# Optimization experiments

Hardware: AMD Instinct MI355X
Metric: run time of the kernel (lower is better)

## Reference

```python
import jax, jax.numpy as jnp
import numpy as np

MAX_ANGLES = 6
SCALES = 2
BN_EPS = 1e-5


def _gauss(k):
    # Gaussian filter init used by WaveletTransform1D (kernel_size k, sigma=k/4)
    xs = np.arange(k, dtype=np.float32) - k // 2
    w = np.exp(-xs ** 2 / (2.0 * (k / 4.0) ** 2)).astype(np.float32)
    return jnp.asarray((w / w.sum()).reshape(1, 1, k))


def setup_inputs():
    key = jax.random.key(0)
    ks = jax.random.split(key, 8)
    B, C, H, W = 8, 64, 128, 128
    return {
        "x": jax.random.normal(ks[0], (B, C, H, W), jnp.float32),
        "lin1_w": jax.random.normal(ks[1], (32, C * 16), jnp.float32) * 0.02,
        "lin1_b": jnp.zeros((32,), jnp.float32),
        "lin2_w": jax.random.normal(ks[2], (MAX_ANGLES, 32), jnp.float32) * 0.02,
        "lin2_b": jnp.zeros((MAX_ANGLES,), jnp.float32),
        "wf0": _gauss(3),
        "wf1": _gauss(5),
        "fuse_w": jax.random.normal(ks[3], (C, C * SCALES), jnp.float32) * 0.05,
        "fuse_b": jax.random.normal(ks[4], (C,), jnp.float32) * 0.05,
        "bn_gamma": jnp.ones((C,), jnp.float32),
        "bn_beta": jnp.zeros((C,), jnp.float32),
        "bn_mean": jnp.zeros((C,), jnp.float32),
        "bn_var": jnp.ones((C,), jnp.float32),
    }


def _grid_sample(img, grid):
    # torch F.grid_sample, bilinear, align_corners=True, padding_mode='zeros'
    N, C, H, W = img.shape
    ix = (grid[..., 0] + 1.0) * 0.5 * (W - 1)  # (N,Hg,Wg)
    iy = (grid[..., 1] + 1.0) * 0.5 * (H - 1)
    x0 = jnp.floor(ix)
    y0 = jnp.floor(iy)
    wx = ix - x0
    wy = iy - y0

    def gather(xi, yi):
        valid = (xi >= 0) & (xi <= W - 1) & (yi >= 0) & (yi <= H - 1)
        xc = jnp.clip(xi, 0, W - 1).astype(jnp.int32)
        yc = jnp.clip(yi, 0, H - 1).astype(jnp.int32)
        v = jax.vmap(lambda im, yy, xx: im[:, yy, xx])(img, yc, xc)  # (N,C,Hg,Wg)
        return v * valid[:, None, :, :].astype(img.dtype)

    v00 = gather(x0, y0)
    v01 = gather(x0 + 1, y0)
    v10 = gather(x0, y0 + 1)
    v11 = gather(x0 + 1, y0 + 1)
    return (v00 * ((1 - wx) * (1 - wy))[:, None]
            + v01 * (wx * (1 - wy))[:, None]
            + v10 * ((1 - wx) * wy)[:, None]
            + v11 * (wx * wy)[:, None])


def _interp1d(x, Lout):
    # F.interpolate mode='linear', align_corners=False, over last axis
    Lin = x.shape[-1]
    real = jnp.clip((jnp.arange(Lout, dtype=jnp.float32) + 0.5) * (Lin / Lout) - 0.5, 0.0, Lin - 1.0)
    i0 = jnp.floor(real).astype(jnp.int32)
    i1 = jnp.minimum(i0 + 1, Lin - 1)
    w = real - i0
    return x[..., i0] * (1.0 - w) + x[..., i1] * w


def _interp_last_ac(x, Lout):
    # linear interp over last axis, align_corners=True
    Lin = x.shape[-1]
    if Lin == Lout:
        return x
    pos = jnp.arange(Lout, dtype=jnp.float32) * ((Lin - 1) / (Lout - 1))
    i0 = jnp.floor(pos).astype(jnp.int32)
    i1 = jnp.minimum(i0 + 1, Lin - 1)
    w = pos - i0
    return x[..., i0] * (1.0 - w) + x[..., i1] * w


def _avgpool1(x):
    L = x.shape[-1]
    return x[..., : (L // 2) * 2].reshape(x.shape[:-1] + (L // 2, 2)).mean(-1)


def _conv1(sig, w):
    # sig (N,1,L), w (1,1,k), 'same' padding cross-correlation (matches torch Conv1d)
    k = w.shape[-1]
    return jax.lax.conv_general_dilated(sig, w, (1,), [(k // 2, k // 2)],
                                        dimension_numbers=("NCH", "OIH", "NCH"))


def reference(x, lin1_w, lin1_b, lin2_w, lin2_b, wf0, wf1, fuse_w, fuse_b,
              bn_gamma, bn_beta, bn_mean, bn_var):
    B, C, H, W = x.shape
    K = MAX_ANGLES
    # --- AnglePredictor: adaptive avg pool 4x4 (H,W divisible by 4) + MLP ---
    pooled = x.reshape(B, C, 4, H // 4, 4, W // 4).mean(axis=(3, 5))  # (B,C,4,4)
    feat = pooled.reshape(B, C * 16)
    h = jax.nn.relu(feat @ lin1_w.T + lin1_b)
    off = (h @ lin2_w.T + lin2_b) * 30.0
    base = jnp.linspace(0.0, 180.0, K)
    angles = jnp.sort(jnp.clip(base[None, :] + off, 0.0, 180.0), axis=1)  # (B,K)
    # --- RadonTransform: per-angle rotation grid + grid_sample + sum over W ---
    xs = jnp.linspace(-1.0, 1.0, W)
    ys = jnp.linspace(-1.0, 1.0, H)
    yc, xc = jnp.meshgrid(ys, xs, indexing="ij")
    th = angles * (jnp.pi / 180.0)
    co = jnp.cos(th)[:, :, None, None]
    si = jnp.sin(th)[:, :, None, None]
    gx = xc[None, None] * co + yc[None, None] * si
    gy = -xc[None, None] * si + yc[None, None] * co
    grid = jnp.stack([gx, gy], axis=-1).reshape(B * K, H, W, 2)
    xexp = jnp.broadcast_to(x[:, None], (B, K, C, H, W)).reshape(B * K, C, H, W)
    rotated = _grid_sample(xexp, grid)          # (B*K,C,H,W)
    sig = rotated.sum(axis=3)                   # (B*K,C,H) == sinogram permuted
    # --- WaveletTransform1D (2 scales, L=H=128 > 4) ---
    N = B * K
    c0 = _conv1(sig.reshape(N * C, 1, H), wf0).reshape(N, C, H)
    cur = _avgpool1(sig)                        # (N,C,H//2)
    L2 = H // 2
    f1 = _conv1(cur.reshape(N * C, 1, L2), wf1)
    u1 = _interp1d(_avgpool1(f1), L2).reshape(N, C, L2)
    c1 = _interp1d(u1, H)                       # resized to target length H
    coeffs = jnp.stack([c0, c1], axis=2)        # (N,C,SCALES,H)
    wav = coeffs.reshape(B, K, C, SCALES, H).transpose(0, 2, 4, 3, 1)  # (B,C,H,S,K)
    combined = wav.reshape(B, C * SCALES, H, K)  # matches torch .view on contiguous
    # --- bilinear align_corners=True resize (H,K)->(H,W), separable ---
    combined = _interp_last_ac(combined, W)
    combined = _interp_last_ac(combined.swapaxes(-1, -2), H).swapaxes(-1, -2)
    # --- fusion: 1x1 conv + BatchNorm(eval) + ReLU ---
    out = jnp.einsum("oc,bchw->bohw", fuse_w, combined) + fuse_b[None, :, None, None]
    scale = (bn_gamma / jnp.sqrt(bn_var + BN_EPS))[None, :, None, None]
    out = (out - bn_mean[None, :, None, None]) * scale + bn_beta[None, :, None, None]
    return jax.nn.relu(out)
```

## Files before the change

kernel.cpp:

```cpp
#include <hip/hip_runtime.h>
#include <hip/hip_fp16.h>
#include <math.h>

#define BB 8
#define CC 64
#define HH 128
#define WW 128
#define KK 6

#define FEAT_OFF 0
#define COEF_OFF 8192

#define WSTR 133
#define NROW 132
#define IMGW (NROW * WSTR)
#define IBASE (2 * WSTR + 2)

typedef __fp16   h2  __attribute__((ext_vector_type(2)));
typedef _Float16 hf2 __attribute__((ext_vector_type(2)));

#if __has_builtin(__builtin_amdgcn_fdot2)
#define FDOT2(A, B) __builtin_amdgcn_fdot2(__builtin_bit_cast(hf2, (A)), \
                                           __builtin_bit_cast(hf2, (B)), 0.f, false)
#define FDOT2A(A, B, C) __builtin_amdgcn_fdot2(__builtin_bit_cast(hf2, (A)), \
                                               __builtin_bit_cast(hf2, (B)), (C), false)
#define HAVE_FDOT2 1
#endif

__global__ __launch_bounds__(256) void k_pool(const float* __restrict__ x,
                                              float* __restrict__ ws) {
    int bc = blockIdx.x;
    int b = bc >> 6, c = bc & 63;
    int t = threadIdx.x;
    __shared__ float pool_l[16];
    if (t < 16) pool_l[t] = 0.f;
    __syncthreads();
    const float4* img4 = (const float4*)(x + (size_t)bc * 16384);
    float acc[4] = {0.f, 0.f, 0.f, 0.f};
    int cb = (t & 31) >> 3;
    #pragma unroll
    for (int r = 0; r < 16; ++r) {
        float4 v = img4[r * 256 + t];
        acc[r >> 2] += (v.x + v.y) + (v.z + v.w);
    }
    #pragma unroll
    for (int rb = 0; rb < 4; ++rb)
        atomicAdd(&pool_l[rb * 4 + cb], acc[rb]);
    __syncthreads();
    if (t < 16)
        ws[FEAT_OFF + b * 1024 + c * 16 + t] = pool_l[t] * (1.0f / 1024.0f);
}

#ifdef HAVE_FDOT2
#define SAMPLED(RR, CC, ACC) do {                                  \
    float fr_ = floorf(RR), fc_ = floorf(CC);                      \
    float wr_ = (RR) - fr_, wc_ = (CC) - fc_;                      \
    h2 wv_ = __builtin_amdgcn_cvt_pkrtz(1.0f - wc_, wc_);          \
    int idx_ = IBASE + (int)fmaf(fr_, 133.f, fc_);                 \
    h2 tp_ = imgh[idx_];                                           \
    h2 bt_ = imgh[idx_ + WSTR];                                    \
    float top_ = FDOT2(wv_, tp_);                                  \
    float d_ = FDOT2A(wv_, bt_, -top_);                            \
    ACC = fmaf(wr_, d_, ACC + top_);                               \
} while (0)
#else
#define SAMPLED(RR, CC, ACC) do {                                  \
    float fr_ = floorf(RR), fc_ = floorf(CC);                      \
    float wr_ = (RR) - fr_, wc_ = (CC) - fc_;                      \
    int idx_ = IBASE + (int)fmaf(fr_, 133.f, fc_);                 \
    h2 tp_ = imgh[idx_];                                           \
    h2 bt_ = imgh[idx_ + WSTR];                                    \
    float t0_ = fmaf(wc_, (float)tp_.y - (float)tp_.x, (float)tp_.x); \
    float t1_ = fmaf(wc_, (float)bt_.y - (float)bt_.x, (float)bt_.x); \
    ACC += fmaf(wr_, t1_ - t0_, t0_);                              \
} while (0)
#endif

__device__ __forceinline__ void line_bounds(float co, float si, float ix0,
                                            float iy0, int& wA, int& wB) {
    float ic = 1.0f / co, is = 1.0f / (-si);
    float a1 = (-1.0f - ix0) * ic, a2 = (128.0f - ix0) * ic;
    float b1 = (-1.0f - iy0) * is, b2 = (128.0f - iy0) * is;
    float wlo = fmaxf(fminf(a1, a2), fminf(b1, b2));
    float whi = fminf(fmaxf(a1, a2), fmaxf(b1, b2));
    wA = max((int)ceilf(fmaxf(fminf(wlo, 200.f), -200.f)), 0);
    wB = min((int)floorf(fmaxf(fminf(whi, 200.f), -200.f)), 127);
    while (wA <= wB) {
        float cx = fmaf((float)wA, co, ix0), ry = fmaf((float)wA, -si, iy0);
        if (cx >= -1.f && cx <= 128.f && ry >= -1.f && ry <= 128.f) break;
        ++wA;
    }
    while (wB >= wA) {
        float cx = fmaf((float)wB, co, ix0), ry = fmaf((float)wB, -si, iy0);
        if (cx >= -1.f && cx <= 128.f && ry >= -1.f && ry <= 128.f) break;
        --wB;
    }
}

__global__ __launch_bounds__(512)
__attribute__((amdgpu_waves_per_eu(4, 4)))
void k_radon(const float* __restrict__ x,
             const float* __restrict__ lin1_w,
             const float* __restrict__ lin1_b,
             const float* __restrict__ lin2_w,
             const float* __restrict__ lin2_b,
             const float* __restrict__ wf0,
             const float* __restrict__ wf1,
             float* __restrict__ ws) {
    int bc = blockIdx.x;
    int b = bc >> 6, c = bc & 63;
    int t = threadIdx.x;
    __shared__ h2 imgh[IMGW];
    __shared__ float sigl[768];
    __shared__ float feat_l[8 * 132];
    __shared__ float h_l[32];
    __shared__ float ang_l[6], ang_s[6];
    __shared__ float co_l[6], si_l[6];

    const h2 z2 = {(__fp16)0.f, (__fp16)0.f};
    for (int i = t; i < 2 * WSTR; i += 512) {
        imgh[i] = z2;
        imgh[130 * WSTR + i] = z2;
    }
    if (t < 128) {
        h2* r = imgh + (t + 2) * WSTR;
        r[0] = z2;
        r[130] = z2;
    }
    const float4* src4 = (const float4*)(x + (size_t)bc * 16384);
    for (int i = t; i < 4096; i += 512) {
        float4 v = src4[i];
        float nxt = __shfl_down(v.x, 1);
        int j = i & 31, row = i >> 5;
        if (j == 31) nxt = 0.f;
        h2* d = imgh + (row + 2) * WSTR + (j << 2) + 2;
        d[0] = __builtin_amdgcn_cvt_pkrtz(v.x, v.y);
        d[1] = __builtin_amdgcn_cvt_pkrtz(v.y, v.z);
        d[2] = __builtin_amdgcn_cvt_pkrtz(v.z, v.w);
        d[3] = __builtin_amdgcn_cvt_pkrtz(v.w, nxt);
        if (j == 0)
            imgh[(row + 2) * WSTR + 1] = __builtin_amdgcn_cvt_pkrtz(0.f, v.x);
    }
    const float* feat = ws + FEAT_OFF + b * 1024;
    for (int i = t; i < 1024; i += 512)
        feat_l[(i >> 7) * 132 + (i & 127)] = feat[i];
    __syncthreads();
    if (t < 256) {
        int m = t >> 3, part = t & 7;
        const float4* wrow = (const float4*)(lin1_w + m * 1024 + part * 128);
        const float4* frow = (const float4*)(feat_l + part * 132);
        float acc = 0.f;
        #pragma unroll 8
        for (int i = 0; i < 32; ++i) {
            float4 wv = wrow[i], fv = frow[i];
            acc = fmaf(wv.x, fv.x, acc); acc = fmaf(wv.y, fv.y, acc);
            acc = fmaf(wv.z, fv.z, acc); acc = fmaf(wv.w, fv.w, acc);
        }
        acc += __shfl_xor(acc, 1);
        acc += __shfl_xor(acc, 2);
        acc += __shfl_xor(acc, 4);
        if (part == 0) h_l[m] = fmaxf(acc + lin1_b[m], 0.f);
    }
    __syncthreads();
    if (t < 6) {
        float a = lin2_b[t];
        #pragma unroll
        for (int i = 0; i < 32; ++i) a = fmaf(h_l[i], lin2_w[t * 32 + i], a);
        a = 36.0f * (float)t + a * 30.0f;
        ang_l[t] = fminf(fmaxf(a, 0.f), 180.f);
    }
    __syncthreads();
    if (t == 0) {
        float v[6];
        #pragma unroll
        for (int i = 0; i < 6; ++i) v[i] = ang_l[i];
        for (int i = 1; i < 6; ++i) {
            float key = v[i]; int j = i - 1;
            while (j >= 0 && v[j] > key) { v[j + 1] = v[j]; --j; }
            v[j + 1] = key;
        }
        #pragma unroll
        for (int i = 0; i < 6; ++i) ang_s[i] = v[i];
    }
    __syncthreads();
    if (t < 6) {
        float th = ang_s[t] * (3.14159265358979323846f / 180.0f);
        co_l[t] = cosf(th);
        si_l[t] = sinf(th);
    }
    __syncthreads();

    auto radon_line = [&](float co, float si, float ix0, float iy0,
                          int sA, int sB) -> float {
        int n = sB - sA + 1;
        if (n <= 0) return 0.f;
        float rr0 = fmaf((float)sA, -si, iy0);
        float cc0 = fmaf((float)sA,  co, ix0);
        float rr1 = rr0 - si, cc1 = cc0 + co;
        float rr2 = rr1 - si, cc2 = cc1 + co;
        float rr3 = rr2 - si, cc3 = cc2 + co;
        float si4 = 4.0f * si, co4 = 4.0f * co;
        float a0 = 0.f, a1 = 0.f, a2 = 0.f, a3 = 0.f;
        int i = n;
        while (i >= 4) {
            SAMPLED(rr0, cc0, a0);
            SAMPLED(rr1, cc1, a1);
            SAMPLED(rr2, cc2, a2);
            SAMPLED(rr3, cc3, a3);
            rr0 -= si4; cc0 += co4;
            rr1 -= si4; cc1 += co4;
            rr2 -= si4; cc2 += co4;
            rr3 -= si4; cc3 += co4;
            i -= 4;
        }
        if (i > 0) SAMPLED(rr0, cc0, a0);
        if (i > 1) SAMPLED(rr1, cc1, a1);
        if (i > 2) SAMPLED(rr2, cc2, a2);
        return (a0 + a1) + (a2 + a3);
    };

    {
        int p = t, k = p >> 7, h = p & 127;
        float co = co_l[k], si = si_l[k];
        float yc = fmaf((float)h, 2.0f / 127.0f, -1.0f);
        float ix0 = (fmaf(yc, si, -co) + 1.0f) * 63.5f;
        float iy0 = (fmaf(yc, co,  si) + 1.0f) * 63.5f;
        int wA, wB;
        line_bounds(co, si, ix0, iy0, wA, wB);
        sigl[p] = radon_line(co, si, ix0, iy0, wA, wB);
    }
    {
        int p = 512 + (t >> 1), k = p >> 7, h = p & 127;
        int half = t & 1;
        float co = co_l[k], si = si_l[k];
        float yc = fmaf((float)h, 2.0f / 127.0f, -1.0f);
        float ix0 = (fmaf(yc, si, -co) + 1.0f) * 63.5f;
        float iy0 = (fmaf(yc, co,  si) + 1.0f) * 63.5f;
        int wA, wB;
        line_bounds(co, si, ix0, iy0, wA, wB);
        int mid = wA + ((wB - wA + 1) >> 1);
        int sA = half ? mid : wA;
        int sB = half ? wB : (mid - 1);
        float a = radon_line(co, si, ix0, iy0, sA, sB);
        a += __shfl_xor(a, 1);
        if (half == 0) sigl[p] = a;
    }
    __syncthreads();

    float* scr = (float*)imgh;
    float* cur = scr;
    float* f1  = scr + 384;
    float* p1  = scr + 768;
    float* u1  = scr + 960;
    float g0 = wf0[0], g1 = wf0[1], g2 = wf0[2];

    for (int p = t; p < 768; p += 512) {
        int k = p >> 7, h = p & 127;
        const float* s = sigl + k * 128;
        float sm1 = (h > 0)   ? s[h - 1] : 0.f;
        float sp1 = (h < 127) ? s[h + 1] : 0.f;
        float c0 = sm1 * g0 + s[h] * g1 + sp1 * g2;
        ws[COEF_OFF + (((b * 6 + k) * 64 + c) * 2 + 0) * 128 + h] = c0;
    }
    for (int q = t; q < 384; q += 512) {
        int k = q >> 6, l = q & 63;
        cur[q] = (sigl[k * 128 + 2 * l] + sigl[k * 128 + 2 * l + 1]) * 0.5f;
    }
    __syncthreads();

    float w10 = wf1[0], w11 = wf1[1], w12 = wf1[2], w13 = wf1[3], w14 = wf1[4];
    for (int q = t; q < 384; q += 512) {
        int k = q >> 6, l = q & 63;
        const float* cu = cur + k * 64;
        float a = cu[l] * w12;
        a += (l >= 2)  ? cu[l - 2] * w10 : 0.f;
        a += (l >= 1)  ? cu[l - 1] * w11 : 0.f;
        a += (l <= 62) ? cu[l + 1] * w13 : 0.f;
        a += (l <= 61) ? cu[l + 2] * w14 : 0.f;
        f1[q] = a;
    }
    __syncthreads();

    for (int q = t; q < 192; q += 512) {
        int k = q >> 5, m = q & 31;
        p1[q] = (f1[k * 64 + 2 * m] + f1[k * 64 + 2 * m + 1]) * 0.5f;
    }
    __syncthreads();

    for (int q = t; q < 384; q += 512) {
        int k = q >> 6, l = q & 63;
        float real = fminf(fmaxf(0.5f * (float)l - 0.25f, 0.f), 31.f);
        int i0 = (int)real;
        int i1 = min(i0 + 1, 31);
        float wv = real - (float)i0;
        u1[q] = p1[k * 32 + i0] * (1.f - wv) + p1[k * 32 + i1] * wv;
    }
    __syncthreads();

    for (int p = t; p < 768; p += 512) {
        int k = p >> 7, h = p & 127;
        float real = fminf(fmaxf(0.5f * (float)h - 0.25f, 0.f), 63.f);
        int i0 = (int)real;
        int i1 = min(i0 + 1, 63);
        float wv = real - (float)i0;
        float c1 = u1[k * 64 + i0] * (1.f - wv) + u1[k * 64 + i1] * wv;
        ws[COEF_OFF + (((b * 6 + k) * 64 + c) * 2 + 1) * 128 + h] = c1;
    }
}

__global__ __launch_bounds__(256, 4) void k_fuseout(const float* __restrict__ fuse_w,
                                                    const float* __restrict__ fuse_b,
                                                    const float* __restrict__ bn_gamma,
                                                    const float* __restrict__ bn_beta,
                                                    const float* __restrict__ bn_mean,
                                                    const float* __restrict__ bn_var,
                                                    const float* __restrict__ ws,
                                                    float* __restrict__ out) {
    int blk = blockIdx.x;
    int b = blk >> 7, oq = (blk >> 5) & 3, j = blk & 31;
    int t = threadIdx.x;
    __shared__ float M_l[6 * 128 * 4];
    __shared__ float W_l[16 * 132];
    __shared__ float P_l[4 * 16 * 4 * 6];
    __shared__ float S_l[16 * 4 * 6];

    for (int i = t; i < 1536; i += 256) {
        int half = i & 1, s = (i >> 1) & 1, cc = (i >> 2) & 63, k = i >> 8;
        const float* src = ws + COEF_OFF +
            (((b * 6 + k) * 64 + cc) * 2 + s) * 128 + half * 64 + 2 * j;
        float v0 = src[0], v1 = src[1];
        int c2 = 2 * cc + half;
        float* d = M_l + (k * 128 + c2) * 4;
        d[s] = v0;
        d[2 + s] = v1;
    }
    for (int i = t; i < 2048; i += 256) {
        int op = i >> 7, c2 = i & 127;
        W_l[op * 132 + c2] = fuse_w[(oq * 16 + op) * 128 + c2];
    }
    __syncthreads();

    int cq = t >> 6, op = (t >> 2) & 15, h2p = t & 3;
    {
        float acc[6] = {0.f, 0.f, 0.f, 0.f, 0.f, 0.f};
        const float* wrow = W_l + op * 132 + cq * 32;
        const float* mbase = M_l + (cq * 32) * 4 + h2p;
        #pragma unroll 4
        for (int c2 = 0; c2 < 32; ++c2) {
            float wv = wrow[c2];
            const float* m = mbase + c2 * 4;
            #pragma unroll
            for (int k = 0; k < 6; ++k)
                acc[k] = fmaf(wv, m[k * 512], acc[k]);
        }
        float* prow = P_l + ((cq * 16 + op) * 4 + h2p) * 6;
        #pragma unroll
        for (int k = 0; k < 6; ++k)
            prow[k] = acc[k];
    }
    __syncthreads();

    if (cq == 0) {
        int o = oq * 16 + op;
        float scale = bn_gamma[o] * rsqrtf(bn_var[o] + 1e-5f);
        float shift = (fuse_b[o] - bn_mean[o]) * scale + bn_beta[o];
        int base = (op * 4 + h2p) * 6;
        float* srow = S_l + base;
        #pragma unroll
        for (int k = 0; k < 6; ++k) {
            float v = P_l[base + k] + P_l[384 + base + k]
                    + P_l[768 + base + k] + P_l[1152 + base + k];
            srow[k] = fmaf(v, scale, shift);
        }
    }
    __syncthreads();

    for (int it = 0; it < 32; ++it) {
        int flat = it * 256 + t;
        int w = flat & 127, row = flat >> 7;
        float pos = (float)w * (5.0f / 127.0f);
        int i0 = min((int)pos, 5);
        int i1 = min(i0 + 1, 5);
        float tt = pos - (float)i0;
        const float* srow = S_l + row * 6;
        float val = srow[i0] * (1.f - tt) + srow[i1] * tt;
        int o = oq * 16 + (row >> 2);
        int h2 = 4 * j + (row & 3);
        out[(((b * 64 + o) * 128) + h2) * 128 + w] = fmaxf(val, 0.f);
    }
}

extern "C" void kernel_launch(void* const* d_in, const int* in_sizes, int n_in,
                              void* d_out, int out_size, void* d_ws, size_t ws_size,
                              hipStream_t stream) {
    const float* x        = (const float*)d_in[0];
    const float* lin1_w   = (const float*)d_in[1];
    const float* lin1_b   = (const float*)d_in[2];
    const float* lin2_w   = (const float*)d_in[3];
    const float* lin2_b   = (const float*)d_in[4];
    const float* wf0      = (const float*)d_in[5];
    const float* wf1      = (const float*)d_in[6];
    const float* fuse_w   = (const float*)d_in[7];
    const float* fuse_b   = (const float*)d_in[8];
    const float* bn_gamma = (const float*)d_in[9];
    const float* bn_beta  = (const float*)d_in[10];
    const float* bn_mean  = (const float*)d_in[11];
    const float* bn_var   = (const float*)d_in[12];
    float* ws  = (float*)d_ws;
    float* out = (float*)d_out;

    hipLaunchKernelGGL(k_pool,    dim3(BB * CC), dim3(256), 0, stream, x, ws);
    hipLaunchKernelGGL(k_radon,   dim3(BB * CC), dim3(512), 0, stream,
                       x, lin1_w, lin1_b, lin2_w, lin2_b, wf0, wf1, ws);
    hipLaunchKernelGGL(k_fuseout, dim3(1024),    dim3(256), 0, stream,
                       fuse_w, fuse_b, bn_gamma, bn_beta, bn_mean, bn_var,
                       ws, out);
}
```

Measured before the change: 163.5 us.

## Pack two channels per half2 in shared image and split angles across blocks

The shared image now packs the same pixel from two adjacent channels into one half2 word, replacing the previous packing of horizontally adjacent pixels. Bilinear sampling is done with packed half arithmetic, so one set of coordinate and weight computations serves two channels. Each block handles a channel pair and half of the six angles, with four threads splitting each line. Interpolation now runs in fp16 instead of fp32 dot products, which costs some precision, and each block loads two images, so it does more global reads and conversions per sample.

New measurement: 167.4 us. 1.02x slower.

```diff
diff --git a/kernel.cpp b/kernel.cpp
--- a/kernel.cpp
+++ b/kernel.cpp
@@ -11,21 +11,12 @@
 #define FEAT_OFF 0
 #define COEF_OFF 8192
 
-#define WSTR 133
-#define NROW 132
-#define IMGW (NROW * WSTR)
-#define IBASE (2 * WSTR + 2)
+#define PSTR 132
+#define PIMG (PSTR * PSTR)
+#define PBASE 0
 
 typedef __fp16   h2  __attribute__((ext_vector_type(2)));
 typedef _Float16 hf2 __attribute__((ext_vector_type(2)));
-
-#if __has_builtin(__builtin_amdgcn_fdot2)
-#define FDOT2(A, B) __builtin_amdgcn_fdot2(__builtin_bit_cast(hf2, (A)), \
-                                           __builtin_bit_cast(hf2, (B)), 0.f, false)
-#define FDOT2A(A, B, C) __builtin_amdgcn_fdot2(__builtin_bit_cast(hf2, (A)), \
-                                               __builtin_bit_cast(hf2, (B)), (C), false)
-#define HAVE_FDOT2 1
-#endif
 
 __global__ __launch_bounds__(256) void k_pool(const float* __restrict__ x,
                                               float* __restrict__ ws) {
@@ -51,30 +42,22 @@
         ws[FEAT_OFF + b * 1024 + c * 16 + t] = pool_l[t] * (1.0f / 1024.0f);
 }
 
-#ifdef HAVE_FDOT2
-#define SAMPLED(RR, CC, ACC) do {                                  \
+#define SAMPLEP(RR, CC, AA, AB) do {                               \
     float fr_ = floorf(RR), fc_ = floorf(CC);                      \
     float wr_ = (RR) - fr_, wc_ = (CC) - fc_;                      \
-    h2 wv_ = __builtin_amdgcn_cvt_pkrtz(1.0f - wc_, wc_);          \
-    int idx_ = IBASE + (int)fmaf(fr_, 133.f, fc_);                 \
-    h2 tp_ = imgh[idx_];                                           \
-    h2 bt_ = imgh[idx_ + WSTR];                                    \
-    float top_ = FDOT2(wv_, tp_);                                  \
-    float d_ = FDOT2A(wv_, bt_, -top_);                            \
-    ACC = fmaf(wr_, d_, ACC + top_);                               \
+    hf2 wc2_ = __builtin_bit_cast(hf2, __builtin_amdgcn_cvt_pkrtz(wc_, wc_)); \
+    hf2 wr2_ = __builtin_bit_cast(hf2, __builtin_amdgcn_cvt_pkrtz(wr_, wr_)); \
+    int idx_ = (int)fmaf(fr_, 132.f, fc_);                         \
+    hf2 l0_ = __builtin_bit_cast(hf2, imgp[idx_]);                 \
+    hf2 l1_ = __builtin_bit_cast(hf2, imgp[idx_ + PSTR]);          \
+    hf2 r0_ = __builtin_bit_cast(hf2, imgp[idx_ + 1]);             \
+    hf2 r1_ = __builtin_bit_cast(hf2, imgp[idx_ + PSTR + 1]);      \
+    hf2 top_ = l0_ + wc2_ * (r0_ - l0_);                           \
+    hf2 bot_ = l1_ + wc2_ * (r1_ - l1_);                           \
+    hf2 mid_ = top_ + wr2_ * (bot_ - top_);                        \
+    AA += (float)mid_.x;                                           \
+    AB += (float)mid_.y;                                           \
 } while (0)
-#else
-#define SAMPLED(RR, CC, ACC) do {                                  \
-    float fr_ = floorf(RR), fc_ = floorf(CC);                      \
-    float wr_ = (RR) - fr_, wc_ = (CC) - fc_;                      \
-    int idx_ = IBASE + (int)fmaf(fr_, 133.f, fc_);                 \
-    h2 tp_ = imgh[idx_];                                           \
-    h2 bt_ = imgh[idx_ + WSTR];                                    \
-    float t0_ = fmaf(wc_, (float)tp_.y - (float)tp_.x, (float)tp_.x); \
-    float t1_ = fmaf(wc_, (float)bt_.y - (float)bt_.x, (float)bt_.x); \
-    ACC += fmaf(wr_, t1_ - t0_, t0_);                              \
-} while (0)
-#endif
 
 __device__ __forceinline__ void line_bounds(float co, float si, float ix0,
                                             float iy0, int& wA, int& wB) {
@@ -98,7 +81,6 @@
 }
 
 __global__ __launch_bounds__(512)
-__attribute__((amdgpu_waves_per_eu(4, 4)))
 void k_radon(const float* __restrict__ x,
              const float* __restrict__ lin1_w,
              const float* __restrict__ lin1_b,
@@ -107,39 +89,35 @@
              const float* __restrict__ wf0,
              const float* __restrict__ wf1,
              float* __restrict__ ws) {
-    int bc = blockIdx.x;
-    int b = bc >> 6, c = bc & 63;
+    int blk = blockIdx.x;
+    int b = blk >> 6, j = (blk >> 1) & 31, ha = blk & 1;
     int t = threadIdx.x;
-    __shared__ h2 imgh[IMGW];
+    __shared__ unsigned imgp[PIMG];
     __shared__ float sigl[768];
     __shared__ float feat_l[8 * 132];
     __shared__ float h_l[32];
     __shared__ float ang_l[6], ang_s[6];
     __shared__ float co_l[6], si_l[6];
 
-    const h2 z2 = {(__fp16)0.f, (__fp16)0.f};
-    for (int i = t; i < 2 * WSTR; i += 512) {
-        imgh[i] = z2;
-        imgh[130 * WSTR + i] = z2;
-    }
-    if (t < 128) {
-        h2* r = imgh + (t + 2) * WSTR;
-        r[0] = z2;
-        r[130] = z2;
-    }
-    const float4* src4 = (const float4*)(x + (size_t)bc * 16384);
+    for (int i = t; i < 2 * PSTR; i += 512) {
+        imgp[i] = 0u;
+        imgp[130 * PSTR + i] = 0u;
+    }
+    {
+        int r = 2 + (t >> 2), sel = t & 3;
+        int col = (sel < 2) ? sel : (128 + sel);
+        imgp[r * PSTR + col] = 0u;
+    }
+    const float4* A4 = (const float4*)(x + (size_t)((b << 6) + (j << 1)) * 16384);
+    const float4* B4 = A4 + 4096;
     for (int i = t; i < 4096; i += 512) {
-        float4 v = src4[i];
-        float nxt = __shfl_down(v.x, 1);
-        int j = i & 31, row = i >> 5;
-        if (j == 31) nxt = 0.f;
-        h2* d = imgh + (row + 2) * WSTR + (j << 2) + 2;
-        d[0] = __builtin_amdgcn_cvt_pkrtz(v.x, v.y);
-        d[1] = __builtin_amdgcn_cvt_pkrtz(v.y, v.z);
-        d[2] = __builtin_amdgcn_cvt_pkrtz(v.z, v.w);
-        d[3] = __builtin_amdgcn_cvt_pkrtz(v.w, nxt);
-        if (j == 0)
-            imgh[(row + 2) * WSTR + 1] = __builtin_amdgcn_cvt_pkrtz(0.f, v.x);
+        float4 va = A4[i], vb = B4[i];
+        int m4 = i & 31, row = i >> 5;
+        unsigned* d = imgp + (row + 2) * PSTR + (m4 << 2) + 2;
+        d[0] = __builtin_bit_cast(unsigned, __builtin_amdgcn_cvt_pkrtz(va.x, vb.x));
+        d[1] = __builtin_bit_cast(unsigned, __builtin_amdgcn_cvt_pkrtz(va.y, vb.y));
+        d[2] = __builtin_bit_cast(unsigned, __builtin_amdgcn_cvt_pkrtz(va.z, vb.z));
+        d[3] = __builtin_bit_cast(unsigned, __builtin_amdgcn_cvt_pkrtz(va.w, vb.w));
     }
     const float* feat = ws + FEAT_OFF + b * 1024;
     for (int i = t; i < 1024; i += 512)
@@ -175,9 +153,9 @@
         #pragma unroll
         for (int i = 0; i < 6; ++i) v[i] = ang_l[i];
         for (int i = 1; i < 6; ++i) {
-            float key = v[i]; int j = i - 1;
-            while (j >= 0 && v[j] > key) { v[j + 1] = v[j]; --j; }
-            v[j + 1] = key;
+            float key = v[i]; int jj = i - 1;
+            while (jj >= 0 && v[jj] > key) { v[jj + 1] = v[jj]; --jj; }
+            v[jj + 1] = key;
         }
         #pragma unroll
         for (int i = 0; i < 6; ++i) ang_s[i] = v[i];
@@ -190,88 +168,92 @@
     }
     __syncthreads();
 
-    auto radon_line = [&](float co, float si, float ix0, float iy0,
-                          int sA, int sB) -> float {
+    auto radon_line2 = [&](float co, float si, float ix0s, float iy0s,
+                           int sA, int sB, float& oA, float& oB) {
+        float a0A = 0.f, a1A = 0.f, a2A = 0.f, a3A = 0.f;
+        float a0B = 0.f, a1B = 0.f, a2B = 0.f, a3B = 0.f;
         int n = sB - sA + 1;
-        if (n <= 0) return 0.f;
-        float rr0 = fmaf((float)sA, -si, iy0);
-        float cc0 = fmaf((float)sA,  co, ix0);
-        float rr1 = rr0 - si, cc1 = cc0 + co;
-        float rr2 = rr1 - si, cc2 = cc1 + co;
-        float rr3 = rr2 - si, cc3 = cc2 + co;
-        float si4 = 4.0f * si, co4 = 4.0f * co;
-        float a0 = 0.f, a1 = 0.f, a2 = 0.f, a3 = 0.f;
-        int i = n;
-        while (i >= 4) {
-            SAMPLED(rr0, cc0, a0);
-            SAMPLED(rr1, cc1, a1);
-            SAMPLED(rr2, cc2, a2);
-            SAMPLED(rr3, cc3, a3);
-            rr0 -= si4; cc0 += co4;
-            rr1 -= si4; cc1 += co4;
-            rr2 -= si4; cc2 += co4;
-            rr3 -= si4; cc3 += co4;
-            i -= 4;
-        }
-        if (i > 0) SAMPLED(rr0, cc0, a0);
-        if (i > 1) SAMPLED(rr1, cc1, a1);
-        if (i > 2) SAMPLED(rr2, cc2, a2);
-        return (a0 + a1) + (a2 + a3);
+        if (n > 0) {
+            float rr0 = fmaf((float)sA, -si, iy0s);
+            float cc0 = fmaf((float)sA,  co, ix0s);
+            float rr1 = rr0 - si, cc1 = cc0 + co;
+            float rr2 = rr1 - si, cc2 = cc1 + co;
+            float rr3 = rr2 - si, cc3 = cc2 + co;
+            float si4 = 4.0f * si, co4 = 4.0f * co;
+            int i = n;
+            while (i >= 4) {
+                SAMPLEP(rr0, cc0, a0A, a0B);
+                SAMPLEP(rr1, cc1, a1A, a1B);
+                SAMPLEP(rr2, cc2, a2A, a2B);
+                SAMPLEP(rr3, cc3, a3A, a3B);
+                rr0 -= si4; cc0 += co4;
+                rr1 -= si4; cc1 += co4;
+                rr2 -= si4; cc2 += co4;
+                rr3 -= si4; cc3 += co4;
+                i -= 4;
+            }
+            if (i > 0) SAMPLEP(rr0, cc0, a0A, a0B);
+            if (i > 1) SAMPLEP(rr1, cc1, a1A, a1B);
+            if (i > 2) SAMPLEP(rr2, cc2, a2A, a2B);
+        }
+        oA = (a0A + a1A) + (a2A + a3A);
+        oB = (a0B + a1B) + (a2B + a3B);
     };
 
-    {
-        int p = t, k = p >> 7, h = p & 127;
-        float co = co_l[k], si = si_l[k];
+    int ha3 = ha * 3;
+    #pragma unroll 1
+    for (int q = 0; q < 3; ++q) {
+        int h = t >> 2, qt = t & 3;
+        int kg = ha3 + q;
+        float co = co_l[kg], si = si_l[kg];
         float yc = fmaf((float)h, 2.0f / 127.0f, -1.0f);
         float ix0 = (fmaf(yc, si, -co) + 1.0f) * 63.5f;
         float iy0 = (fmaf(yc, co,  si) + 1.0f) * 63.5f;
         int wA, wB;
         line_bounds(co, si, ix0, iy0, wA, wB);
-        sigl[p] = radon_line(co, si, ix0, iy0, wA, wB);
-    }
-    {
-        int p = 512 + (t >> 1), k = p >> 7, h = p & 127;
-        int half = t & 1;
-        float co = co_l[k], si = si_l[k];
-        float yc = fmaf((float)h, 2.0f / 127.0f, -1.0f);
-        float ix0 = (fmaf(yc, si, -co) + 1.0f) * 63.5f;
-        float iy0 = (fmaf(yc, co,  si) + 1.0f) * 63.5f;
-        int wA, wB;
-        line_bounds(co, si, ix0, iy0, wA, wB);
-        int mid = wA + ((wB - wA + 1) >> 1);
-        int sA = half ? mid : wA;
-        int sB = half ? wB : (mid - 1);
-        float a = radon_line(co, si, ix0, iy0, sA, sB);
-        a += __shfl_xor(a, 1);
-        if (half == 0) sigl[p] = a;
-    }
-    __syncthreads();
-
-    float* scr = (float*)imgh;
+        int len = wB - wA + 1; if (len < 0) len = 0;
+        int s0 = wA + ((len * qt) >> 2);
+        int s1 = wA + ((len * (qt + 1)) >> 2) - 1;
+        float aA, aB;
+        radon_line2(co, si, ix0 + 2.0f, iy0 + 2.0f, s0, s1, aA, aB);
+        aA += __shfl_xor(aA, 1);
+        aA += __shfl_xor(aA, 2);
+        aB += __shfl_xor(aB, 1);
+        aB += __shfl_xor(aB, 2);
+        if (qt == 0) {
+            sigl[(q << 8) + h] = aA;
+            sigl[(q << 8) + 128 + h] = aB;
+        }
+    }
+    __syncthreads();
+
+    float* scr = (float*)imgp;
     float* cur = scr;
     float* f1  = scr + 384;
     float* p1  = scr + 768;
     float* u1  = scr + 960;
     float g0 = wf0[0], g1 = wf0[1], g2 = wf0[2];
+    int c2j = j << 1;
 
     for (int p = t; p < 768; p += 512) {
-        int k = p >> 7, h = p & 127;
-        const float* s = sigl + k * 128;
+        int r = p >> 7, h = p & 127;
+        const float* s = sigl + r * 128;
         float sm1 = (h > 0)   ? s[h - 1] : 0.f;
         float sp1 = (h < 127) ? s[h + 1] : 0.f;
         float c0 = sm1 * g0 + s[h] * g1 + sp1 * g2;
-        ws[COEF_OFF + (((b * 6 + k) * 64 + c) * 2 + 0) * 128 + h] = c0;
+        int kg = ha3 + (r >> 1), cc = c2j + (r & 1);
+        ws[COEF_OFF + (((b * 6 + kg) * 64 + cc) * 2 + 0) * 128 + h] = c0;
     }
     for (int q = t; q < 384; q += 512) {
-        int k = q >> 6, l = q & 63;
-        cur[q] = (sigl[k * 128 + 2 * l] + sigl[k * 128 + 2 * l + 1]) * 0.5f;
+        int r = q >> 6, l = q & 63;
+        cur[q] = (sigl[r * 128 + 2 * l] + sigl[r * 128 + 2 * l + 1]) * 0.5f;
     }
     __syncthreads();
 
     float w10 = wf1[0], w11 = wf1[1], w12 = wf1[2], w13 = wf1[3], w14 = wf1[4];
     for (int q = t; q < 384; q += 512) {
-        int k = q >> 6, l = q & 63;
-        const float* cu = cur + k * 64;
+        int r = q >> 6, l = q & 63;
+        const float* cu = cur + r * 64;
         float a = cu[l] * w12;
         a += (l >= 2)  ? cu[l - 2] * w10 : 0.f;
         a += (l >= 1)  ? cu[l - 1] * w11 : 0.f;
@@ -282,29 +264,30 @@
     __syncthreads();
 
     for (int q = t; q < 192; q += 512) {
-        int k = q >> 5, m = q & 31;
-        p1[q] = (f1[k * 64 + 2 * m] + f1[k * 64 + 2 * m + 1]) * 0.5f;
+        int r = q >> 5, m = q & 31;
+        p1[q] = (f1[r * 64 + 2 * m] + f1[r * 64 + 2 * m + 1]) * 0.5f;
     }
     __syncthreads();
 
     for (int q = t; q < 384; q += 512) {
-        int k = q >> 6, l = q & 63;
+        int r = q >> 6, l = q & 63;
         float real = fminf(fmaxf(0.5f * (float)l - 0.25f, 0.f), 31.f);
         int i0 = (int)real;
         int i1 = min(i0 + 1, 31);
         float wv = real - (float)i0;
-        u1[q] = p1[k * 32 + i0] * (1.f - wv) + p1[k * 32 + i1] * wv;
+        u1[q] = p1[r * 32 + i0] * (1.f - wv) + p1[r * 32 + i1] * wv;
     }
     __syncthreads();
 
     for (int p = t; p < 768; p += 512) {
-        int k = p >> 7, h = p & 127;
+        int r = p >> 7, h = p & 127;
         float real = fminf(fmaxf(0.5f * (float)h - 0.25f, 0.f), 63.f);
         int i0 = (int)real;
         int i1 = min(i0 + 1, 63);
         float wv = real - (float)i0;
-        float c1 = u1[k * 64 + i0] * (1.f - wv) + u1[k * 64 + i1] * wv;
-        ws[COEF_OFF + (((b * 6 + k) * 64 + c) * 2 + 1) * 128 + h] = c1;
+        float c1 = u1[r * 64 + i0] * (1.f - wv) + u1[r * 64 + i1] * wv;
+        int kg = ha3 + (r >> 1), cc = c2j + (r & 1);
+        ws[COEF_OFF + (((b * 6 + kg) * 64 + cc) * 2 + 1) * 128 + h] = c1;
     }
 }
 
```
